# Performance work log

Measured on AMD Instinct MI355X. Metric: run time of the kernel, lower is better.

The kernel has to match this reference:

```python
import jax, jax.numpy as jnp
import numpy as np

N = 8192


def setup_inputs() -> dict:
    key = jax.random.key(0)
    k1, k2 = jax.random.split(key)
    X = jax.random.normal(k1, (N,), dtype=jnp.float32)
    X_hat = jax.random.normal(k2, (N,), dtype=jnp.float32)
    return {"X": X, "X_hat": X_hat}


def reference(X, X_hat):
    n = X.shape[0]
    # Faithful to the torch module: compare argsort indices (not ranks)
    # over the full i,j meshgrid ('ij' indexing == broadcasting below).
    a = jnp.argsort(X)        # [n] int
    b = jnp.argsort(X_hat)    # [n] int
    ai, aj = a[:, None], a[None, :]   # [n,1], [1,n]
    bi, bj = b[:, None], b[None, :]
    disordered = ((ai < aj) & (bi > bj)) | ((ai > aj) & (bi < bj))  # [n,n] bool
    ndisordered = jnp.sum(disordered)
    return ndisordered.astype(jnp.float32) / (n * (n - 1))
```

## Files before the change

kernel.cpp:

```cpp
#include <hip/hip_runtime.h>

#define KN 8192

__device__ __forceinline__ unsigned long long make_key(float x, int idx) {
    unsigned int u = __float_as_uint(x);
    u ^= (unsigned int)((int)u >> 31) | 0x80000000u;
    return ((unsigned long long)u << 13) | (unsigned int)idx;
}

constexpr int UT  = 1024;
constexpr int VC  = 128;
constexpr int NVT = KN / VC;

__global__ __launch_bounds__(256) void rank_partial(const float* __restrict__ X,
                                                    const float* __restrict__ Xh,
                                                    int* __restrict__ part) {
    int blk = blockIdx.x;
    int arr = blk & 1;
    int vt  = (blk >> 1) & (NVT - 1);
    int ut  = blk >> 7;
    const float* src = arr ? Xh : X;

    int tid = threadIdx.x;
    int u0 = ut * UT + tid;

    unsigned long long ku0 = make_key(src[u0],       u0);
    unsigned long long ku1 = make_key(src[u0 + 256], u0 + 256);
    unsigned long long ku2 = make_key(src[u0 + 512], u0 + 512);
    unsigned long long ku3 = make_key(src[u0 + 768], u0 + 768);

    __shared__ unsigned long long tile[VC];
    if (tid < VC) {
        int v = vt * VC + tid;
        tile[tid] = make_key(src[v], v);
    }
    __syncthreads();

    int c0 = 0, c1 = 0, c2 = 0, c3 = 0;
#pragma unroll 8
    for (int jj = 0; jj < VC; ++jj) {
        unsigned long long kv = tile[jj];
        c0 += (kv < ku0);
        c1 += (kv < ku1);
        c2 += (kv < ku2);
        c3 += (kv < ku3);
    }

    int base = (arr * NVT + vt) * KN + u0;
    part[base]       = c0;
    part[base + 256] = c1;
    part[base + 512] = c2;
    part[base + 768] = c3;
}

__global__ __launch_bounds__(256) void reduce_scatter(const int* __restrict__ part,
                                                      int* __restrict__ a,
                                                      int* __restrict__ b) {
    int t = blockIdx.x * 256 + threadIdx.x;
    int arr = t >> 13;
    int u   = t & (KN - 1);

    const int* p = part + (arr * NVT) * KN + u;
    int r = 0;
#pragma unroll 8
    for (int vt = 0; vt < NVT; ++vt) r += p[vt * KN];

    if (arr == 0) a[r] = u; else b[r] = u;
}

__global__ __launch_bounds__(256) void gather_e(const int* __restrict__ a,
                                                const int* __restrict__ b,
                                                int* __restrict__ e) {
    int i = blockIdx.x * 256 + threadIdx.x;
    e[a[i]] = b[i];
}

__global__ __launch_bounds__(256) void inv_count(const int* __restrict__ e,
                                                 int* __restrict__ inv_part) {
    constexpr int TS = 256;
    constexpr int T  = KN / TS;

    int blk = blockIdx.x;
    int p = 0, rem = blk;
    while (rem >= T - p) { rem -= T - p; ++p; }
    int q = p + rem;

    __shared__ int le[TS];
    __shared__ int wsum[4];
    int tid = threadIdx.x;

    int ek = e[p * TS + tid];
    le[tid] = e[q * TS + tid];
    __syncthreads();

    int cnt = 0;
    if (p == q) {
        for (int j = tid + 1; j < TS; ++j) cnt += (ek > le[j]);
    } else {
        const int4* le4 = (const int4*)le;
#pragma unroll 8
        for (int j4 = 0; j4 < TS / 4; ++j4) {
            int4 v = le4[j4];
            cnt += (ek > v.x) + (ek > v.y) + (ek > v.z) + (ek > v.w);
        }
    }

    for (int off = 32; off; off >>= 1) cnt += __shfl_down(cnt, off);
    if ((tid & 63) == 0) wsum[tid >> 6] = cnt;
    __syncthreads();
    if (tid == 0) inv_part[blk] = wsum[0] + wsum[1] + wsum[2] + wsum[3];
}

__global__ __launch_bounds__(256) void finalize_k(const int* __restrict__ inv_part,
                                                  float* __restrict__ out) {
    __shared__ int wsum[4];
    int tid = threadIdx.x;
    int cnt = 0;
    for (int i = tid; i < 528; i += 256) cnt += inv_part[i];
    for (int off = 32; off; off >>= 1) cnt += __shfl_down(cnt, off);
    if ((tid & 63) == 0) wsum[tid >> 6] = cnt;
    __syncthreads();
    if (tid == 0) {
        float D = (float)(wsum[0] + wsum[1] + wsum[2] + wsum[3]);
        out[0] = 2.0f * D / ((float)KN * (float)(KN - 1));
    }
}

extern "C" void kernel_launch(void* const* d_in, const int* in_sizes, int n_in,
                              void* d_out, int out_size, void* d_ws, size_t ws_size,
                              hipStream_t stream) {
    const float* X  = (const float*)d_in[0];
    const float* Xh = (const float*)d_in[1];

    char* ws = (char*)d_ws;
    int* part     = (int*)(ws);
    int* a        = (int*)(ws + 4194304);
    int* b        = (int*)(ws + 4227072);
    int* e        = (int*)(ws + 4259840);
    int* inv_part = (int*)(ws + 4292608);

    rank_partial  <<<dim3(1024), dim3(256), 0, stream>>>(X, Xh, part);
    reduce_scatter<<<dim3(64),   dim3(256), 0, stream>>>(part, a, b);
    gather_e      <<<dim3(32),   dim3(256), 0, stream>>>(a, b, e);
    inv_count     <<<dim3(528),  dim3(256), 0, stream>>>(e, inv_part);
    finalize_k    <<<dim3(1),    dim3(256), 0, stream>>>(inv_part, (float*)d_out);
}
```

Before: 78.63 us.

## Fuse gather and finalize into inversion kernel with atomic last-block reduction

Drops the gather_e kernel by storing each element's rank of X and indexing b through it directly inside the inversion-count kernel. Drops the finalize kernel by having each block atomically add its count to a global counter, with the last block (via a ticket counter) writing the output. This cuts two kernel launches and their serialization gaps, at the cost of a double-indirect gather per load and atomic traffic on a single counter. The counters are reset inside reduce_scatter, which relies on stream ordering.

```diff
diff --git a/kernel.cpp b/kernel.cpp
--- a/kernel.cpp
+++ b/kernel.cpp
@@ -54,8 +54,12 @@
 }
 
 __global__ __launch_bounds__(256) void reduce_scatter(const int* __restrict__ part,
-                                                      int* __restrict__ a,
-                                                      int* __restrict__ b) {
+                                                      int* __restrict__ rank_a,
+                                                      int* __restrict__ b,
+                                                      unsigned int* __restrict__ count,
+                                                      unsigned int* __restrict__ ticket) {
+    if (blockIdx.x == 0 && threadIdx.x == 0) { *count = 0u; *ticket = 0u; }
+
     int t = blockIdx.x * 256 + threadIdx.x;
     int arr = t >> 13;
     int u   = t & (KN - 1);
@@ -65,18 +69,15 @@
 #pragma unroll 8
     for (int vt = 0; vt < NVT; ++vt) r += p[vt * KN];
 
-    if (arr == 0) a[r] = u; else b[r] = u;
+    if (arr == 0) rank_a[u] = r;
+    else          b[r] = u;
 }
 
-__global__ __launch_bounds__(256) void gather_e(const int* __restrict__ a,
-                                                const int* __restrict__ b,
-                                                int* __restrict__ e) {
-    int i = blockIdx.x * 256 + threadIdx.x;
-    e[a[i]] = b[i];
-}
-
-__global__ __launch_bounds__(256) void inv_count(const int* __restrict__ e,
-                                                 int* __restrict__ inv_part) {
+__global__ __launch_bounds__(256) void inv_finalize(const int* __restrict__ rank_a,
+                                                    const int* __restrict__ b,
+                                                    unsigned int* __restrict__ count,
+                                                    unsigned int* __restrict__ ticket,
+                                                    float* __restrict__ out) {
     constexpr int TS = 256;
     constexpr int T  = KN / TS;
 
@@ -89,8 +90,8 @@
     __shared__ int wsum[4];
     int tid = threadIdx.x;
 
-    int ek = e[p * TS + tid];
-    le[tid] = e[q * TS + tid];
+    int ek = b[rank_a[p * TS + tid]];
+    le[tid] = b[rank_a[q * TS + tid]];
     __syncthreads();
 
     int cnt = 0;
@@ -108,21 +109,16 @@
     for (int off = 32; off; off >>= 1) cnt += __shfl_down(cnt, off);
     if ((tid & 63) == 0) wsum[tid >> 6] = cnt;
     __syncthreads();
-    if (tid == 0) inv_part[blk] = wsum[0] + wsum[1] + wsum[2] + wsum[3];
-}
 
-__global__ __launch_bounds__(256) void finalize_k(const int* __restrict__ inv_part,
-                                                  float* __restrict__ out) {
-    __shared__ int wsum[4];
-    int tid = threadIdx.x;
-    int cnt = 0;
-    for (int i = tid; i < 528; i += 256) cnt += inv_part[i];
-    for (int off = 32; off; off >>= 1) cnt += __shfl_down(cnt, off);
-    if ((tid & 63) == 0) wsum[tid >> 6] = cnt;
-    __syncthreads();
     if (tid == 0) {
-        float D = (float)(wsum[0] + wsum[1] + wsum[2] + wsum[3]);
-        out[0] = 2.0f * D / ((float)KN * (float)(KN - 1));
+        unsigned int blkCnt = (unsigned int)(wsum[0] + wsum[1] + wsum[2] + wsum[3]);
+        atomicAdd(count, blkCnt);
+        __threadfence();
+        unsigned int done = atomicAdd(ticket, 1u);
+        if (done == 527u) {
+            unsigned int D = atomicAdd(count, 0u);
+            out[0] = 2.0f * (float)D / ((float)KN * (float)(KN - 1));
+        }
     }
 }
 
@@ -133,15 +129,14 @@
     const float* Xh = (const float*)d_in[1];
 
     char* ws = (char*)d_ws;
-    int* part     = (int*)(ws);
-    int* a        = (int*)(ws + 4194304);
-    int* b        = (int*)(ws + 4227072);
-    int* e        = (int*)(ws + 4259840);
-    int* inv_part = (int*)(ws + 4292608);
+    int* part            = (int*)(ws);
+    int* rank_a          = (int*)(ws + 4194304);
+    int* b               = (int*)(ws + 4227072);
+    unsigned int* count  = (unsigned int*)(ws + 4259840);
+    unsigned int* ticket = (unsigned int*)(ws + 4259844);
 
     rank_partial  <<<dim3(1024), dim3(256), 0, stream>>>(X, Xh, part);
-    reduce_scatter<<<dim3(64),   dim3(256), 0, stream>>>(part, a, b);
-    gather_e      <<<dim3(32),   dim3(256), 0, stream>>>(a, b, e);
-    inv_count     <<<dim3(528),  dim3(256), 0, stream>>>(e, inv_part);
-    finalize_k    <<<dim3(1),    dim3(256), 0, stream>>>(inv_part, (float*)d_out);
+    reduce_scatter<<<dim3(64),   dim3(256), 0, stream>>>(part, rank_a, b, count, ticket);
+    inv_finalize  <<<dim3(528),  dim3(256), 0, stream>>>(rank_a, b, count, ticket,
+                                                         (float*)d_out);
 }
```

Result: slower. 83.89 us (+6.7%).
